# Performance work log

Measured on AMD Instinct MI355X. Metric: run time of the kernel, lower is better.

## Reference

```python
import itertools
import jax, jax.numpy as jnp
import numpy as np

N_QUBITS = 8
N_LAYERS = 2
BATCH = 8192
INPUT_DIM = 3072
NUM_CLASSES = 10

_In = np.eye(2, dtype=np.complex64)
_Xn = np.array([[0, 1], [1, 0]], dtype=np.complex64)
_Yn = np.array([[0, -1j], [1j, 0]], dtype=np.complex64)
_Zn = np.array([[1, 0], [0, -1]], dtype=np.complex64)
_P = {"I": _In, "X": _Xn, "Y": _Yn, "Z": _Zn}
_XX = jnp.asarray(np.kron(_Xn, _Xn))
_YY = jnp.asarray(np.kron(_Yn, _Yn))
_ZZ = jnp.asarray(np.kron(_Zn, _Zn))
_I4 = jnp.eye(4, dtype=jnp.complex64)
# 2-qubit Pauli words in PennyLane ArbitraryUnitary order: IX, IY, IZ, XI, ..., ZZ
_WORDS = jnp.asarray(np.stack([np.kron(_P[a], _P[b]) for a, b in itertools.product("IXYZ", repeat=2)][1:]))


def apply_gate(state, U, wires):
    """Apply a 2^k x 2^k gate U to the given wires of a (2,)*n statevector."""
    n = state.ndim
    k = len(wires)
    U = U.reshape((2,) * (2 * k)).astype(state.dtype)
    state = jnp.tensordot(U, state, axes=(list(range(k, 2 * k)), list(wires)))
    rest = [a for a in range(n) if a not in wires]
    perm = [0] * n
    for i, a in enumerate(wires):
        perm[a] = i
    for j, a in enumerate(rest):
        perm[a] = k + j
    return jnp.transpose(state, perm)


def u3_mat(t, p, d):
    ct, st = jnp.cos(t / 2).astype(jnp.complex64), jnp.sin(t / 2).astype(jnp.complex64)
    r0 = jnp.stack([ct, -jnp.exp(1j * d) * st])
    r1 = jnp.stack([jnp.exp(1j * p) * st, jnp.exp(1j * (p + d)) * ct])
    return jnp.stack([r0, r1])


def ry_mat(t):
    c, s = jnp.cos(t / 2), jnp.sin(t / 2)
    return jnp.stack([jnp.stack([c, -s]), jnp.stack([s, c])]).astype(jnp.complex64)


def ising_mat(phi, pauli2):
    # exp(-i phi/2 P) for two-qubit Pauli word P (P^2 = I)
    return jnp.cos(phi / 2) * _I4 - 1j * jnp.sin(phi / 2) * pauli2


def circuit(conv_w, pool_w, last_w, feats):
    state = jnp.zeros((2,) * N_QUBITS, jnp.complex64).at[(0,) * N_QUBITS].set(1.0)
    # AngleEmbedding with RY rotations
    for w in range(N_QUBITS):
        state = apply_gate(state, ry_mat(feats[w]), (w,))
    wires = list(range(N_QUBITS))
    for layer in range(N_LAYERS):
        cw = conv_w[layer]
        nw = len(wires)
        for p in (0, 1):
            for idx in range(nw - 1):
                if idx % 2 == p:
                    a, b = wires[idx], wires[idx + 1]
                    state = apply_gate(state, u3_mat(cw[idx, 0], cw[idx, 1], cw[idx, 2]), (a,))
                    state = apply_gate(state, u3_mat(cw[idx + 1, 3], cw[idx + 1, 4], cw[idx + 1, 5]), (b,))
                    state = apply_gate(state, ising_mat(cw[idx, 6], _ZZ), (a, b))
                    state = apply_gate(state, ising_mat(cw[idx, 7], _YY), (a, b))
                    state = apply_gate(state, ising_mat(cw[idx, 8], _XX), (a, b))
                    state = apply_gate(state, u3_mat(cw[idx, 9], cw[idx, 10], cw[idx, 11]), (a,))
                    state = apply_gate(state, u3_mat(cw[idx + 1, 12], cw[idx + 1, 13], cw[idx + 1, 14]), (b,))
        # Pooling: mid-circuit measure + conditional U3 == (deferred measurement)
        pw = pool_w[layer]
        for idx in range(1, nw, 2):
            u = u3_mat(pw[idx // 2, 0], pw[idx // 2, 1], pw[idx // 2, 2])
            cu = jnp.zeros((4, 4), jnp.complex64).at[0, 0].set(1.0).at[1, 1].set(1.0).at[2:, 2:].set(u)
            state = apply_gate(state, cu, (wires[idx], wires[idx - 1]))
        wires = wires[::2]
    # ArbitraryUnitary on remaining 2 wires: product of 15 PauliRot gates
    for k in range(15):
        mat = jnp.cos(last_w[k] / 2) * _I4 - 1j * jnp.sin(last_w[k] / 2) * _WORDS[k]
        state = apply_gate(state, mat, tuple(wires))
    probs = state.real ** 2 + state.imag ** 2
    z = jnp.sum(probs, axis=tuple(range(1, N_QUBITS)))  # (2,)
    return z[0] - z[1]


def setup_inputs() -> dict:
    key = jax.random.key(0)
    ks = jax.random.split(key, 8)
    return {
        "x": jax.random.normal(ks[0], (BATCH, INPUT_DIM), jnp.float32),
        "fc_w": jax.random.normal(ks[1], (N_QUBITS, INPUT_DIM), jnp.float32) * 0.02,
        "fc_b": jnp.zeros((N_QUBITS,), jnp.float32),
        "conv_params": jax.random.normal(ks[2], (N_LAYERS, N_QUBITS, 15), jnp.float32),
        "pool_params": jax.random.normal(ks[3], (N_LAYERS, N_QUBITS // 2, 3), jnp.float32),
        "last_params": jax.random.normal(ks[4], (15,), jnp.float32),
        "out_w": jax.random.normal(ks[5], (NUM_CLASSES, 1), jnp.float32),
        "out_b": jnp.zeros((NUM_CLASSES,), jnp.float32),
    }


def reference(x, fc_w, fc_b, conv_params, pool_params, last_params, out_w, out_b):
    feats = jnp.tanh(x.reshape(x.shape[0], -1) @ fc_w.T + fc_b)  # (B, n_qubits)
    qvals = jax.vmap(lambda f: circuit(conv_params, pool_params, last_params, f))(feats)
    logits = qvals[:, None].astype(x.dtype) @ out_w.T + out_b  # (B, num_classes)
    return logits
```

## Files before the change

kernel.cpp:

```cpp
#include <hip/hip_runtime.h>
#include <math.h>

__constant__ int G_ORD[17] = {0,1,2,3,4,5,6, 10,11,12,13, 7,8,9, 14,15, 16};
__constant__ int G_WA[17]  = {0,2,4,6,1,3,5, 1,3,5,7, 0,4,2, 2,6, 0};
__constant__ int G_WB[17]  = {1,3,5,7,2,4,6, 0,2,4,6, 2,6,4, 0,4, 4};
__constant__ int CDESC[10][3] = {{0,0,1},{0,2,3},{0,4,5},{0,6,7},{0,1,2},{0,3,4},{0,5,6},
                                 {1,0,1},{1,2,3},{1,1,2}};
__constant__ int PDESC[6][2] = {{0,0},{0,1},{0,2},{0,3},{1,0},{1,1}};
__constant__ float2 PMAT[4][4] = {
  {{1.f,0.f},{0.f,0.f},{0.f,0.f},{1.f,0.f}},
  {{0.f,0.f},{1.f,0.f},{1.f,0.f},{0.f,0.f}},
  {{0.f,0.f},{0.f,-1.f},{0.f,1.f},{0.f,0.f}},
  {{1.f,0.f},{0.f,0.f},{0.f,0.f},{-1.f,0.f}}};

__device__ __forceinline__ float2 cmul(float2 a, float2 b){
  return make_float2(a.x*b.x - a.y*b.y, a.x*b.y + a.y*b.x);
}
__device__ __forceinline__ float2 cadd(float2 a, float2 b){
  return make_float2(a.x+b.x, a.y+b.y);
}

__device__ void u3m(float t, float p, float d, float2* u){
  float ct = cosf(0.5f*t), st = sinf(0.5f*t);
  u[0] = make_float2(ct, 0.f);
  u[1] = make_float2(-cosf(d)*st, -sinf(d)*st);
  u[2] = make_float2(cosf(p)*st,  sinf(p)*st);
  u[3] = make_float2(cosf(p+d)*ct, sinf(p+d)*ct);
}

__device__ void kron2(const float2* A, const float2* B, float2* M){
  #pragma unroll
  for (int ia=0; ia<2; ia++)
    #pragma unroll
    for (int ib=0; ib<2; ib++)
      #pragma unroll
      for (int ja=0; ja<2; ja++)
        #pragma unroll
        for (int jb=0; jb<2; jb++)
          M[(ia*2+ib)*4 + (ja*2+jb)] = cmul(A[ia*2+ja], B[ib*2+jb]);
}

__device__ void mul44(const float2* A, const float2* B, float2* C){
  #pragma unroll
  for (int r=0;r<4;r++)
    #pragma unroll
    for (int c=0;c<4;c++){
      float2 s = make_float2(0.f,0.f);
      #pragma unroll
      for (int k=0;k<4;k++) s = cadd(s, cmul(A[r*4+k], B[k*4+c]));
      C[r*4+c] = s;
    }
}

__device__ void rotword(float phi, int qa, int qb, float2* R){
  float ch = cosf(0.5f*phi), sh = sinf(0.5f*phi);
  float2 W[16];
  kron2(PMAT[qa], PMAT[qb], W);
  #pragma unroll
  for (int i=0;i<16;i++) R[i] = make_float2(sh*W[i].y, -sh*W[i].x);
  #pragma unroll
  for (int d=0;d<4;d++) R[d*4+d].x += ch;
}

__global__ __launch_bounds__(64) void build_gates_kernel(
    const float* __restrict__ conv, const float* __restrict__ pool,
    const float* __restrict__ last, float* __restrict__ gates){
  int t = threadIdx.x;
  float2 M[16], T[16], R[16];
  if (t < 10){
    int layer = CDESC[t][0], ra = CDESC[t][1], rb = CDESC[t][2];
    const float* cw = conv + layer*120;
    int bA = ra*15, bB = rb*15;
    float2 A1[4], B1[4], A2[4], B2[4], K[16];
    u3m(cw[bA+0], cw[bA+1], cw[bA+2], A1);
    u3m(cw[bB+3], cw[bB+4], cw[bB+5], B1);
    kron2(A1, B1, M);
    rotword(cw[bA+6], 3, 3, R); mul44(R, M, T);
    rotword(cw[bA+7], 2, 2, R); mul44(R, T, M);
    rotword(cw[bA+8], 1, 1, R); mul44(R, M, T);
    u3m(cw[bA+9],  cw[bA+10], cw[bA+11], A2);
    u3m(cw[bB+12], cw[bB+13], cw[bB+14], B2);
    kron2(A2, B2, K); mul44(K, T, M);
  } else if (t < 16){
    int layer = PDESC[t-10][0], h = PDESC[t-10][1];
    const float* pw = pool + layer*12 + h*3;
    float2 u[4];
    u3m(pw[0], pw[1], pw[2], u);
    #pragma unroll
    for (int i=0;i<16;i++) M[i] = make_float2(0.f,0.f);
    M[0]  = make_float2(1.f,0.f);
    M[5]  = make_float2(1.f,0.f);
    M[10] = u[0]; M[11] = u[1]; M[14] = u[2]; M[15] = u[3];
  } else if (t == 16){
    #pragma unroll
    for (int i=0;i<16;i++) M[i] = make_float2((i%5==0)?1.f:0.f, 0.f);
    for (int k=0;k<15;k++){
      int w = k+1;
      rotword(last[k], w>>2, w&3, R);
      mul44(R, M, T);
      #pragma unroll
      for (int i=0;i<16;i++) M[i] = T[i];
    }
  }
  if (t < 17){
    float2* dst = (float2*)(gates + t*32);
    #pragma unroll
    for (int i=0;i<16;i++) dst[i] = M[i];
  }
}

__global__ __launch_bounds__(64) void build_u_kernel(
    const float* __restrict__ gates, float2* __restrict__ U){
  __shared__ float2 st[256];
  int lane = threadIdx.x, col = blockIdx.x;
  #pragma unroll
  for (int k=lane; k<256; k+=64) st[k] = make_float2(k==col ? 1.f : 0.f, 0.f);
  __syncthreads();
  for (int g=0; g<17; g++){
    int slot = G_ORD[g];
    const float2* gm = (const float2*)(gates + slot*32);
    float2 m[16];
    #pragma unroll
    for (int i=0;i<16;i++) m[i] = gm[i];
    int pa = 7 - G_WA[g], pb = 7 - G_WB[g];
    int plo = pa < pb ? pa : pb, phi_ = pa < pb ? pb : pa;
    int mm = lane;
    int t1   = ((mm >> plo) << (plo+1)) | (mm & ((1<<plo)-1));
    int base = ((t1 >> phi_) << (phi_+1)) | (t1 & ((1<<phi_)-1));
    int ba = 1<<pa, bb = 1<<pb;
    int i0 = base, i1 = base|bb, i2 = base|ba, i3 = base|ba|bb;
    float2 s0 = st[i0], s1 = st[i1], s2 = st[i2], s3 = st[i3];
    float2 n0 = cadd(cadd(cmul(m[0], s0), cmul(m[1], s1)), cadd(cmul(m[2], s2), cmul(m[3], s3)));
    float2 n1 = cadd(cadd(cmul(m[4], s0), cmul(m[5], s1)), cadd(cmul(m[6], s2), cmul(m[7], s3)));
    float2 n2 = cadd(cadd(cmul(m[8], s0), cmul(m[9], s1)), cadd(cmul(m[10],s2), cmul(m[11],s3)));
    float2 n3 = cadd(cadd(cmul(m[12],s0), cmul(m[13],s1)), cadd(cmul(m[14],s2), cmul(m[15],s3)));
    st[i0] = n0; st[i1] = n1; st[i2] = n2; st[i3] = n3;
    __syncthreads();
  }
  #pragma unroll
  for (int k=lane; k<256; k+=64) U[k*256 + col] = st[k];
}

__global__ __launch_bounds__(256) void build_a_kernel(
    const float2* __restrict__ U, float* __restrict__ A){
  int j = threadIdx.x, i0 = blockIdx.x*4;
  float a0=0.f, a1=0.f, a2=0.f, a3=0.f;
  for (int k=0; k<256; k++){
    float2 uj = U[k*256 + j];
    float2 u0 = U[k*256 + i0+0];
    float2 u1 = U[k*256 + i0+1];
    float2 u2 = U[k*256 + i0+2];
    float2 u3v = U[k*256 + i0+3];
    float sgn = (k < 128) ? 1.f : -1.f;
    a0 += sgn*(u0.x*uj.x + u0.y*uj.y);
    a1 += sgn*(u1.x*uj.x + u1.y*uj.y);
    a2 += sgn*(u2.x*uj.x + u2.y*uj.y);
    a3 += sgn*(u3v.x*uj.x + u3v.y*uj.y);
  }
  A[(i0+0)*256 + j] = a0;
  A[(i0+1)*256 + j] = a1;
  A[(i0+2)*256 + j] = a2;
  A[(i0+3)*256 + j] = a3;
}

__global__ __launch_bounds__(256) void feats_kernel(
    const float* __restrict__ x, const float* __restrict__ fcw,
    const float* __restrict__ fcb, float* __restrict__ feats){
  __shared__ float red[256];
  int t = threadIdx.x, lane = t & 63, wid = t >> 6;
  int row0 = blockIdx.x * 8;
  float w[8][12];
  #pragma unroll
  for (int o=0;o<8;o++){
    const float4* wp = (const float4*)(fcw + o*3072 + t*12);
    float4 w0 = wp[0], w1 = wp[1], w2 = wp[2];
    w[o][0]=w0.x; w[o][1]=w0.y; w[o][2]=w0.z; w[o][3]=w0.w;
    w[o][4]=w1.x; w[o][5]=w1.y; w[o][6]=w1.z; w[o][7]=w1.w;
    w[o][8]=w2.x; w[o][9]=w2.y; w[o][10]=w2.z; w[o][11]=w2.w;
  }
  for (int half=0; half<2; half++){
    float acc[4][8];
    #pragma unroll
    for (int rr=0; rr<4; rr++){
      int row = row0 + half*4 + rr;
      const float4* xp = (const float4*)(x + (size_t)row*3072 + t*12);
      float4 x0 = xp[0], x1 = xp[1], x2 = xp[2];
      float xv[12] = {x0.x,x0.y,x0.z,x0.w, x1.x,x1.y,x1.z,x1.w, x2.x,x2.y,x2.z,x2.w};
      #pragma unroll
      for (int o=0;o<8;o++){
        float s = 0.f;
        #pragma unroll
        for (int j=0;j<12;j++) s += xv[j]*w[o][j];
        acc[rr][o] = s;
      }
    }
    #pragma unroll
    for (int rr=0; rr<4; rr++)
      #pragma unroll
      for (int o=0;o<8;o++){
        float v = acc[rr][o];
        #pragma unroll
        for (int m=1; m<64; m<<=1) v += __shfl_xor(v, m, 64);
        if (lane == 0) red[wid*64 + (half*4+rr)*8 + o] = v;
      }
  }
  __syncthreads();
  if (t < 64){
    float s = red[t] + red[64+t] + red[128+t] + red[192+t];
    int r = t >> 3, o = t & 7;
    feats[(row0+r)*8 + o] = tanhf(s + fcb[o]);
  }
}

__global__ __launch_bounds__(128) void psi_kernel(
    const float* __restrict__ feats, float* __restrict__ psigT){
  int row = blockIdx.x*128 + threadIdx.x;
  float c[8], s[8];
  #pragma unroll
  for (int w=0; w<8; w++){
    float f = 0.5f*feats[row*8 + w];
    c[w] = cosf(f); s[w] = sinf(f);
  }
  float g2[2], g4[4], g8[8], H[16], L[16];
  g2[0]=c[0]; g2[1]=s[0];
  #pragma unroll
  for (int a=0;a<2;a++){ g4[a*2]=g2[a]*c[1]; g4[a*2+1]=g2[a]*s[1]; }
  #pragma unroll
  for (int a=0;a<4;a++){ g8[a*2]=g4[a]*c[2]; g8[a*2+1]=g4[a]*s[2]; }
  #pragma unroll
  for (int a=0;a<8;a++){ H[a*2]=g8[a]*c[3]; H[a*2+1]=g8[a]*s[3]; }
  g2[0]=c[4]; g2[1]=s[4];
  #pragma unroll
  for (int a=0;a<2;a++){ g4[a*2]=g2[a]*c[5]; g4[a*2+1]=g2[a]*s[5]; }
  #pragma unroll
  for (int a=0;a<4;a++){ g8[a*2]=g4[a]*c[6]; g8[a*2+1]=g4[a]*s[6]; }
  #pragma unroll
  for (int a=0;a<8;a++){ L[a*2]=g8[a]*c[7]; L[a*2+1]=g8[a]*s[7]; }
  #pragma unroll
  for (int i=0;i<256;i++)
    psigT[(size_t)i*8192 + row] = H[i>>4]*L[i&15];
}

__global__ __launch_bounds__(256) void qform_kernel(
    const float* __restrict__ Ag, const float* __restrict__ psigT,
    const float* __restrict__ outw, const float* __restrict__ outb,
    float* __restrict__ out){
  __shared__ float As[32*256];
  int t = threadIdx.x;
  int r0 = blockIdx.x * 32;
  int wv = t >> 6, jb = t & 63;
  int w = __builtin_amdgcn_readfirstlane(wv);
  float acc[8][4];
  #pragma unroll
  for (int rr=0;rr<8;rr++){ acc[rr][0]=0.f; acc[rr][1]=0.f; acc[rr][2]=0.f; acc[rr][3]=0.f; }
  for (int chunk=0; chunk<8; chunk++){
    #pragma unroll
    for (int pass=0; pass<8; pass++){
      int kk = pass*4 + wv;
      *(float4*)(As + kk*256 + jb*4) =
        *(const float4*)(Ag + (chunk*32 + kk)*256 + jb*4);
    }
    __syncthreads();
    #pragma unroll 4
    for (int kk=0; kk<32; kk++){
      int k = chunk*32 + kk;
      const float* pr = psigT + (size_t)k*8192 + (r0 + 8*w);
      float4 av = *(const float4*)(As + kk*256 + jb*4);
      #pragma unroll
      for (int rr=0; rr<8; rr++){
        float sv = pr[rr];
        acc[rr][0] += sv*av.x; acc[rr][1] += sv*av.y;
        acc[rr][2] += sv*av.z; acc[rr][3] += sv*av.w;
      }
    }
    __syncthreads();
  }
  float p[8];
  #pragma unroll
  for (int rr=0; rr<8; rr++){
    int row = r0 + 8*w + rr;
    float v0 = psigT[(size_t)(jb*4+0)*8192 + row];
    float v1 = psigT[(size_t)(jb*4+1)*8192 + row];
    float v2 = psigT[(size_t)(jb*4+2)*8192 + row];
    float v3 = psigT[(size_t)(jb*4+3)*8192 + row];
    p[rr] = acc[rr][0]*v0 + acc[rr][1]*v1 + acc[rr][2]*v2 + acc[rr][3]*v3;
  }
  #pragma unroll
  for (int rr=0; rr<8; rr++)
    #pragma unroll
    for (int m=1; m<64; m<<=1) p[rr] += __shfl_xor(p[rr], m, 64);
  if ((t & 63) == 0){
    #pragma unroll
    for (int rr=0; rr<8; rr++){
      int row = r0 + 8*w + rr;
      float q = p[rr];
      #pragma unroll
      for (int c=0; c<10; c++)
        out[row*10 + c] = q*outw[c] + outb[c];
    }
  }
}

extern "C" void kernel_launch(void* const* d_in, const int* in_sizes, int n_in,
                              void* d_out, int out_size, void* d_ws, size_t ws_size,
                              hipStream_t stream) {
  const float* x    = (const float*)d_in[0];
  const float* fcw  = (const float*)d_in[1];
  const float* fcb  = (const float*)d_in[2];
  const float* conv = (const float*)d_in[3];
  const float* pool = (const float*)d_in[4];
  const float* last = (const float*)d_in[5];
  const float* outw = (const float*)d_in[6];
  const float* outb = (const float*)d_in[7];
  float* out = (float*)d_out;

  float* ws = (float*)d_ws;
  float*  gates = ws;
  float2* U     = (float2*)(ws + 1024);
  float*  Am    = ws + 1024 + 131072;
  float*  feats = Am + 65536;
  float*  psigT = feats + 65536;

  build_gates_kernel<<<1, 64, 0, stream>>>(conv, pool, last, gates);
  build_u_kernel<<<256, 64, 0, stream>>>(gates, U);
  build_a_kernel<<<64, 256, 0, stream>>>(U, Am);
  feats_kernel<<<1024, 256, 0, stream>>>(x, fcw, fcb, feats);
  psi_kernel<<<64, 128, 0, stream>>>(feats, psigT);
  qform_kernel<<<256, 256, 0, stream>>>(Am, psigT, outw, outb, out);
}
```

Baseline: 301.2 us.

## Fuse psi construction into qform kernel and restructure feats GEMV reduction

Removes the separate psi kernel and its 8 MB transposed product-state buffer in global memory. Each qform block now rebuilds its 16 rows of the 256-entry product state in shared memory using fast sincos and runs the quadratic form out of LDS. The feats kernel switches to coalesced float4 loads with per-lane partial sums, reduced once through padded shared memory instead of many wave shuffles. build_a is also split across twice as many blocks for more parallelism, at the cost of reloading A from global memory in more qform blocks.

```diff
diff --git a/kernel.cpp b/kernel.cpp
--- a/kernel.cpp
+++ b/kernel.cpp
@@ -143,117 +143,106 @@
 
 __global__ __launch_bounds__(256) void build_a_kernel(
     const float2* __restrict__ U, float* __restrict__ A){
-  int j = threadIdx.x, i0 = blockIdx.x*4;
-  float a0=0.f, a1=0.f, a2=0.f, a3=0.f;
+  int j = threadIdx.x, i0 = blockIdx.x*2;
+  float a0=0.f, a1=0.f;
+  #pragma unroll 8
   for (int k=0; k<256; k++){
     float2 uj = U[k*256 + j];
     float2 u0 = U[k*256 + i0+0];
     float2 u1 = U[k*256 + i0+1];
-    float2 u2 = U[k*256 + i0+2];
-    float2 u3v = U[k*256 + i0+3];
     float sgn = (k < 128) ? 1.f : -1.f;
     a0 += sgn*(u0.x*uj.x + u0.y*uj.y);
     a1 += sgn*(u1.x*uj.x + u1.y*uj.y);
-    a2 += sgn*(u2.x*uj.x + u2.y*uj.y);
-    a3 += sgn*(u3v.x*uj.x + u3v.y*uj.y);
   }
   A[(i0+0)*256 + j] = a0;
   A[(i0+1)*256 + j] = a1;
-  A[(i0+2)*256 + j] = a2;
-  A[(i0+3)*256 + j] = a3;
 }
 
 __global__ __launch_bounds__(256) void feats_kernel(
     const float* __restrict__ x, const float* __restrict__ fcw,
     const float* __restrict__ fcb, float* __restrict__ feats){
-  __shared__ float red[256];
-  int t = threadIdx.x, lane = t & 63, wid = t >> 6;
-  int row0 = blockIdx.x * 8;
-  float w[8][12];
-  #pragma unroll
-  for (int o=0;o<8;o++){
-    const float4* wp = (const float4*)(fcw + o*3072 + t*12);
-    float4 w0 = wp[0], w1 = wp[1], w2 = wp[2];
-    w[o][0]=w0.x; w[o][1]=w0.y; w[o][2]=w0.z; w[o][3]=w0.w;
-    w[o][4]=w1.x; w[o][5]=w1.y; w[o][6]=w1.z; w[o][7]=w1.w;
-    w[o][8]=w2.x; w[o][9]=w2.y; w[o][10]=w2.z; w[o][11]=w2.w;
-  }
-  for (int half=0; half<2; half++){
-    float acc[4][8];
-    #pragma unroll
-    for (int rr=0; rr<4; rr++){
-      int row = row0 + half*4 + rr;
-      const float4* xp = (const float4*)(x + (size_t)row*3072 + t*12);
-      float4 x0 = xp[0], x1 = xp[1], x2 = xp[2];
-      float xv[12] = {x0.x,x0.y,x0.z,x0.w, x1.x,x1.y,x1.z,x1.w, x2.x,x2.y,x2.z,x2.w};
+  __shared__ float red[128*68];
+  int t = threadIdx.x, lane = t & 63, wv = t >> 6;
+  int r0 = blockIdx.x * 16;
+  int rw = r0 + wv*4;
+  const float4* x4 = (const float4*)x;
+  const float4* w4 = (const float4*)fcw;
+  float acc[4][8];
+  #pragma unroll
+  for (int r=0;r<4;r++)
+    #pragma unroll
+    for (int o=0;o<8;o++) acc[r][o] = 0.f;
+  for (int p=0; p<12; p++){
+    float4 wf[8];
+    #pragma unroll
+    for (int o=0;o<8;o++) wf[o] = w4[o*768 + p*64 + lane];
+    #pragma unroll
+    for (int r=0;r<4;r++){
+      float4 xv = x4[(size_t)(rw+r)*768 + p*64 + lane];
       #pragma unroll
       for (int o=0;o<8;o++){
-        float s = 0.f;
-        #pragma unroll
-        for (int j=0;j<12;j++) s += xv[j]*w[o][j];
-        acc[rr][o] = s;
+        acc[r][o] += xv.x*wf[o].x + xv.y*wf[o].y + xv.z*wf[o].z + xv.w*wf[o].w;
       }
     }
-    #pragma unroll
-    for (int rr=0; rr<4; rr++)
-      #pragma unroll
-      for (int o=0;o<8;o++){
-        float v = acc[rr][o];
-        #pragma unroll
-        for (int m=1; m<64; m<<=1) v += __shfl_xor(v, m, 64);
-        if (lane == 0) red[wid*64 + (half*4+rr)*8 + o] = v;
-      }
-  }
+  }
+  #pragma unroll
+  for (int r=0;r<4;r++)
+    #pragma unroll
+    for (int o=0;o<8;o++)
+      red[((wv*4+r)*8 + o)*68 + lane] = acc[r][o];
   __syncthreads();
-  if (t < 64){
-    float s = red[t] + red[64+t] + red[128+t] + red[192+t];
-    int r = t >> 3, o = t & 7;
-    feats[(row0+r)*8 + o] = tanhf(s + fcb[o]);
-  }
-}
-
-__global__ __launch_bounds__(128) void psi_kernel(
-    const float* __restrict__ feats, float* __restrict__ psigT){
-  int row = blockIdx.x*128 + threadIdx.x;
-  float c[8], s[8];
-  #pragma unroll
-  for (int w=0; w<8; w++){
-    float f = 0.5f*feats[row*8 + w];
-    c[w] = cosf(f); s[w] = sinf(f);
-  }
-  float g2[2], g4[4], g8[8], H[16], L[16];
-  g2[0]=c[0]; g2[1]=s[0];
-  #pragma unroll
-  for (int a=0;a<2;a++){ g4[a*2]=g2[a]*c[1]; g4[a*2+1]=g2[a]*s[1]; }
-  #pragma unroll
-  for (int a=0;a<4;a++){ g8[a*2]=g4[a]*c[2]; g8[a*2+1]=g4[a]*s[2]; }
-  #pragma unroll
-  for (int a=0;a<8;a++){ H[a*2]=g8[a]*c[3]; H[a*2+1]=g8[a]*s[3]; }
-  g2[0]=c[4]; g2[1]=s[4];
-  #pragma unroll
-  for (int a=0;a<2;a++){ g4[a*2]=g2[a]*c[5]; g4[a*2+1]=g2[a]*s[5]; }
-  #pragma unroll
-  for (int a=0;a<4;a++){ g8[a*2]=g4[a]*c[6]; g8[a*2+1]=g4[a]*s[6]; }
-  #pragma unroll
-  for (int a=0;a<8;a++){ L[a*2]=g8[a]*c[7]; L[a*2+1]=g8[a]*s[7]; }
-  #pragma unroll
-  for (int i=0;i<256;i++)
-    psigT[(size_t)i*8192 + row] = H[i>>4]*L[i&15];
+  if (t < 128){
+    const float4* rp = (const float4*)(red + t*68);
+    float4 s4 = make_float4(0.f,0.f,0.f,0.f);
+    #pragma unroll
+    for (int i=0;i<16;i++){
+      float4 v = rp[i];
+      s4.x += v.x; s4.y += v.y; s4.z += v.z; s4.w += v.w;
+    }
+    float s = s4.x + s4.y + s4.z + s4.w + fcb[t & 7];
+    feats[(r0 + (t>>3))*8 + (t&7)] = tanhf(s);
+  }
 }
 
 __global__ __launch_bounds__(256) void qform_kernel(
-    const float* __restrict__ Ag, const float* __restrict__ psigT,
+    const float* __restrict__ Ag, const float* __restrict__ feats,
     const float* __restrict__ outw, const float* __restrict__ outb,
     float* __restrict__ out){
   __shared__ float As[32*256];
+  __shared__ float ps[16*256];
   int t = threadIdx.x;
-  int r0 = blockIdx.x * 32;
+  int r0 = blockIdx.x * 16;
+  {
+    int row = t >> 4, i1 = t & 15;
+    const float* f = feats + (r0 + row)*8;
+    float c[8], s[8];
+    #pragma unroll
+    for (int w=0; w<8; w++){
+      float a = 0.5f*f[w];
+      __sincosf(a, &s[w], &c[w]);
+    }
+    float Hv = (i1&8 ? s[0]:c[0]) * (i1&4 ? s[1]:c[1])
+             * (i1&2 ? s[2]:c[2]) * (i1&1 ? s[3]:c[3]);
+    float l2[2], l4[4], l8[8], L[16];
+    l2[0]=c[4]; l2[1]=s[4];
+    #pragma unroll
+    for (int a=0;a<2;a++){ l4[a*2]=l2[a]*c[5]; l4[a*2+1]=l2[a]*s[5]; }
+    #pragma unroll
+    for (int a=0;a<4;a++){ l8[a*2]=l4[a]*c[6]; l8[a*2+1]=l4[a]*s[6]; }
+    #pragma unroll
+    for (int a=0;a<8;a++){ L[a*2]=l8[a]*c[7]; L[a*2+1]=l8[a]*s[7]; }
+    float* dst = ps + row*256 + i1*16;
+    #pragma unroll
+    for (int j=0;j<16;j++) dst[j] = Hv*L[j];
+  }
   int wv = t >> 6, jb = t & 63;
-  int w = __builtin_amdgcn_readfirstlane(wv);
-  float acc[8][4];
-  #pragma unroll
-  for (int rr=0;rr<8;rr++){ acc[rr][0]=0.f; acc[rr][1]=0.f; acc[rr][2]=0.f; acc[rr][3]=0.f; }
+  const float4* As4 = (const float4*)As;
+  const float4* ps4 = (const float4*)ps;
+  float4 acc4[4];
+  #pragma unroll
+  for (int r=0;r<4;r++) acc4[r] = make_float4(0.f,0.f,0.f,0.f);
   for (int chunk=0; chunk<8; chunk++){
+    __syncthreads();
     #pragma unroll
     for (int pass=0; pass<8; pass++){
       int kk = pass*4 + wv;
@@ -261,43 +250,35 @@
         *(const float4*)(Ag + (chunk*32 + kk)*256 + jb*4);
     }
     __syncthreads();
-    #pragma unroll 4
-    for (int kk=0; kk<32; kk++){
-      int k = chunk*32 + kk;
-      const float* pr = psigT + (size_t)k*8192 + (r0 + 8*w);
-      float4 av = *(const float4*)(As + kk*256 + jb*4);
-      #pragma unroll
-      for (int rr=0; rr<8; rr++){
-        float sv = pr[rr];
-        acc[rr][0] += sv*av.x; acc[rr][1] += sv*av.y;
-        acc[rr][2] += sv*av.z; acc[rr][3] += sv*av.w;
+    #pragma unroll
+    for (int kk4=0; kk4<8; kk4++){
+      float4 av0 = As4[(kk4*4+0)*64 + jb];
+      float4 av1 = As4[(kk4*4+1)*64 + jb];
+      float4 av2 = As4[(kk4*4+2)*64 + jb];
+      float4 av3 = As4[(kk4*4+3)*64 + jb];
+      #pragma unroll
+      for (int r=0; r<4; r++){
+        float4 pv = ps4[(wv*4+r)*64 + chunk*8 + kk4];
+        acc4[r].x += pv.x*av0.x + pv.y*av1.x + pv.z*av2.x + pv.w*av3.x;
+        acc4[r].y += pv.x*av0.y + pv.y*av1.y + pv.z*av2.y + pv.w*av3.y;
+        acc4[r].z += pv.x*av0.z + pv.y*av1.z + pv.z*av2.z + pv.w*av3.z;
+        acc4[r].w += pv.x*av0.w + pv.y*av1.w + pv.z*av2.w + pv.w*av3.w;
       }
     }
-    __syncthreads();
-  }
-  float p[8];
-  #pragma unroll
-  for (int rr=0; rr<8; rr++){
-    int row = r0 + 8*w + rr;
-    float v0 = psigT[(size_t)(jb*4+0)*8192 + row];
-    float v1 = psigT[(size_t)(jb*4+1)*8192 + row];
-    float v2 = psigT[(size_t)(jb*4+2)*8192 + row];
-    float v3 = psigT[(size_t)(jb*4+3)*8192 + row];
-    p[rr] = acc[rr][0]*v0 + acc[rr][1]*v1 + acc[rr][2]*v2 + acc[rr][3]*v3;
-  }
-  #pragma unroll
-  for (int rr=0; rr<8; rr++)
-    #pragma unroll
-    for (int m=1; m<64; m<<=1) p[rr] += __shfl_xor(p[rr], m, 64);
-  if ((t & 63) == 0){
-    #pragma unroll
-    for (int rr=0; rr<8; rr++){
-      int row = r0 + 8*w + rr;
-      float q = p[rr];
-      #pragma unroll
-      for (int c=0; c<10; c++)
-        out[row*10 + c] = q*outw[c] + outb[c];
-    }
+  }
+  float p[4];
+  #pragma unroll
+  for (int r=0; r<4; r++){
+    float4 psv = ps4[(wv*4+r)*64 + jb];
+    float pr = acc4[r].x*psv.x + acc4[r].y*psv.y + acc4[r].z*psv.z + acc4[r].w*psv.w;
+    #pragma unroll
+    for (int m=1; m<64; m<<=1) pr += __shfl_xor(pr, m, 64);
+    p[r] = pr;
+  }
+  if (jb < 40){
+    int ridx = jb / 10, c = jb - ridx*10;
+    float q = (ridx==0) ? p[0] : (ridx==1) ? p[1] : (ridx==2) ? p[2] : p[3];
+    out[(r0 + wv*4 + ridx)*10 + c] = q*outw[c] + outb[c];
   }
 }
 
@@ -319,12 +300,10 @@
   float2* U     = (float2*)(ws + 1024);
   float*  Am    = ws + 1024 + 131072;
   float*  feats = Am + 65536;
-  float*  psigT = feats + 65536;
 
   build_gates_kernel<<<1, 64, 0, stream>>>(conv, pool, last, gates);
   build_u_kernel<<<256, 64, 0, stream>>>(gates, U);
-  build_a_kernel<<<64, 256, 0, stream>>>(U, Am);
-  feats_kernel<<<1024, 256, 0, stream>>>(x, fcw, fcb, feats);
-  psi_kernel<<<64, 128, 0, stream>>>(feats, psigT);
-  qform_kernel<<<256, 256, 0, stream>>>(Am, psigT, outw, outb, out);
-}
+  build_a_kernel<<<128, 256, 0, stream>>>(U, Am);
+  feats_kernel<<<512, 256, 0, stream>>>(x, fcw, fcb, feats);
+  qform_kernel<<<512, 256, 0, stream>>>(Am, feats, outw, outb, out);
+}
```

After: 259.0 us. -14.0%, faster.
